# Optimization experiments

Hardware: AMD Instinct MI355X
Metric: run time of the kernel (lower is better)

The kernel has to match this reference:

```python
import jax, jax.numpy as jnp
import numpy as np

B, S, HID = 2, 2048, 2048
H = 16
Q_LORA = 1536
KV_LORA = 512
NOPE = 128
ROPE = 64
VDIM = 128
EPS = 1e-6
THETA = 10000.0
SCALE = 1.0 / np.sqrt(NOPE + ROPE)


def rmsnorm(x, w):
    var = jnp.mean(jnp.square(x), axis=-1, keepdims=True)
    return x * jax.lax.rsqrt(var + EPS) * w


def rotate_half(x):
    x1, x2 = jnp.split(x, 2, axis=-1)
    return jnp.concatenate([-x2, x1], axis=-1)


def setup_inputs() -> dict:
    key = jax.random.key(0)
    ks = jax.random.split(key, 10)
    w = 0.02
    hidden_states = jax.random.normal(ks[0], (B, S, HID), jnp.float32)
    # causal additive mask (bsz, 1, q_len, kv_len)
    causal = jnp.tril(jnp.ones((S, S), jnp.bool_))
    attention_mask = jnp.where(causal, 0.0, jnp.finfo(jnp.float32).min)[None, None].repeat(B, 0)
    position_ids = jnp.broadcast_to(jnp.arange(S, dtype=jnp.int64), (B, S))
    return {
        'hidden_states': hidden_states,
        'attention_mask': attention_mask,
        'q_a_w': jax.random.normal(ks[1], (Q_LORA, HID), jnp.float32) * w,
        'q_a_ln_w': jnp.ones((Q_LORA,), jnp.float32),
        'q_b_rope_w': jax.random.normal(ks[2], (H * ROPE, Q_LORA), jnp.float32) * w,
        'qk_nope_w': jax.random.normal(ks[3], (H * KV_LORA, Q_LORA), jnp.float32) * w,
        'kv_a_w': jax.random.normal(ks[4], (KV_LORA + ROPE, HID), jnp.float32) * w,
        'kv_a_ln_w': jnp.ones((KV_LORA,), jnp.float32),
        'v_b_w': jax.random.normal(ks[5], (H * VDIM, KV_LORA), jnp.float32) * w,
        'o_w': jax.random.normal(ks[6], (HID, H * VDIM), jnp.float32) * w,
        'position_ids': position_ids,
    }


def reference(hidden_states, attention_mask, q_a_w, q_a_ln_w, q_b_rope_w, qk_nope_w,
              kv_a_w, kv_a_ln_w, v_b_w, o_w, position_ids):
    b, s, _ = hidden_states.shape
    # low-rank Q path
    q_a = rmsnorm(hidden_states @ q_a_w.T, q_a_ln_w)                 # (b,s,Q_LORA)
    q_rope = (q_a @ q_b_rope_w.T).reshape(b, s, H, ROPE).transpose(0, 2, 1, 3)  # (b,h,s,rd)
    # compressed KV + shared rope key
    ckv_full = hidden_states @ kv_a_w.T                              # (b,s,KV_LORA+ROPE)
    ckv = rmsnorm(ckv_full[..., :KV_LORA], kv_a_ln_w)                # (b,s,KV_LORA)
    k_rope = ckv_full[..., KV_LORA:]                                 # (b,s,rd)
    # rotary embedding
    inv_freq = 1.0 / (THETA ** (jnp.arange(0, ROPE, 2, dtype=jnp.float32) / ROPE))
    t = jnp.arange(s, dtype=jnp.float32)
    freqs = jnp.outer(t, inv_freq)                                   # (s, rd/2)
    emb = jnp.concatenate([freqs, freqs], axis=-1)                   # (s, rd)
    cos = jnp.cos(emb)[position_ids][:, None]                        # (b,1,s,rd)
    sin = jnp.sin(emb)[position_ids][:, None]
    q_rope = q_rope * cos + rotate_half(q_rope) * sin                # (b,h,s,rd)
    k_rope = k_rope[:, None] * cos + rotate_half(k_rope[:, None]) * sin  # (b,1,s,rd)
    # absorbed nope score: q_a -> (b,h,s,KV_LORA) then vs compressed kv
    nope_q = (q_a @ qk_nope_w.T).reshape(b, s, H, KV_LORA).transpose(0, 2, 1, 3)
    nope_score = jnp.einsum('bhqc,bkc->bhqk', nope_q, ckv)
    rope_score = jnp.einsum('bhqr,bkr->bhqk', q_rope, k_rope[:, 0])
    attn = (nope_score + rope_score) * SCALE + attention_mask
    attn = jax.nn.softmax(attn.astype(jnp.float32), axis=-1).astype(hidden_states.dtype)
    # AV in compressed space, then absorbed v projection
    ctx = jnp.einsum('bhqk,bkc->bhqc', attn, ckv)                    # (b,h,q,KV_LORA)
    v_w = v_b_w.reshape(H, VDIM, KV_LORA)
    out = jnp.einsum('bhqc,hvc->bhqv', ctx, v_w)                     # (b,h,q,VDIM)
    out = out.transpose(0, 2, 1, 3).reshape(b, s, H * VDIM)
    return out @ o_w.T
```

## Files before the change

kernel.cpp:

```cpp
#include <hip/hip_runtime.h>
#include <hip/hip_bf16.h>

typedef __bf16 bf16;
typedef __bf16 bf16x8 __attribute__((ext_vector_type(8)));
typedef float f32x4 __attribute__((ext_vector_type(4)));
typedef float f32x16 __attribute__((ext_vector_type(16)));

#define AS3(p) ((__attribute__((address_space(3))) void*)(p))
#define AS1(p) ((const __attribute__((address_space(1))) void*)(p))
#define GLDS16(g,l) __builtin_amdgcn_global_load_lds(AS1(g), AS3(l), 16, 0, 0)
#define MFMA_BF16(a,b,c) __builtin_amdgcn_mfma_f32_16x16x32_bf16((a),(b),(c),0,0,0)
#define MFMA32(a,b,c) __builtin_amdgcn_mfma_f32_32x32x16_bf16((a),(b),(c),0,0,0)
#define SCHED_FENCE() do { __builtin_amdgcn_sched_barrier(0); asm volatile("" ::: "memory"); } while (0)

constexpr int S_ = 2048;
constexpr int H_ = 16;
constexpr int KVL_ = 512;
constexpr int ROPE_ = 64;
constexpr int VD_ = 128;
constexpr int DQK_ = 576;
constexpr int QKV_N = 2176;
constexpr float SCALE_ = 0.07216878364870323f;

__device__ __forceinline__ bf16 to_bf16(float f) {
    unsigned u = __builtin_bit_cast(unsigned, f);
    unsigned r = u + 0x7FFFu + ((u >> 16) & 1u);
    unsigned short h = (unsigned short)(r >> 16);
    return __builtin_bit_cast(bf16, h);
}

__device__ __forceinline__ unsigned short bf16bits(float f) {
    unsigned u = __builtin_bit_cast(unsigned, f);
    unsigned r = u + 0x7FFFu + ((u >> 16) & 1u);
    return (unsigned short)(r >> 16);
}

__device__ __forceinline__ unsigned cvt_pk_bf16(float lo, float hi) {
    unsigned r;
    asm("v_cvt_pk_bf16_f32 %0, %1, %2" : "=v"(r) : "v"(lo), "v"(hi));
    return r;
}

__global__ void cast_all_kernel(const float* __restrict__ s0, const float* __restrict__ s1,
                                const float* __restrict__ s2, const float* __restrict__ s3,
                                const float* __restrict__ s4, const float* __restrict__ s5,
                                const float* __restrict__ s6,
                                bf16* __restrict__ d0, bf16* __restrict__ d1, bf16* __restrict__ d2,
                                bf16* __restrict__ d3, bf16* __restrict__ d4, bf16* __restrict__ d5,
                                bf16* __restrict__ d6) {
    constexpr long ns[7]  = {8388608L, 3145728L, 1179648L, 1572864L, 12582912L, 1048576L, 4194304L};
    constexpr long pds[7] = {8388608L, 3145728L, 1310720L, 1572864L, 12582912L, 1048576L, 4194304L};
    const int seg = blockIdx.y;
    const float* in = (seg == 0) ? s0 : (seg == 1) ? s1 : (seg == 2) ? s2 : (seg == 3) ? s3
                    : (seg == 4) ? s4 : (seg == 5) ? s5 : s6;
    bf16* out = (seg == 0) ? d0 : (seg == 1) ? d1 : (seg == 2) ? d2 : (seg == 3) ? d3
              : (seg == 4) ? d4 : (seg == 5) ? d5 : d6;
    const long n = ns[seg], pad = pds[seg];
    long i = ((long)blockIdx.x * 256 + threadIdx.x) * 4;
    const long stride = (long)gridDim.x * 256 * 4;
    for (; i < pad; i += stride) {
        if (i < n) {
            float4 v = *(const float4*)(in + i);
            out[i + 0] = to_bf16(v.x); out[i + 1] = to_bf16(v.y);
            out[i + 2] = to_bf16(v.z); out[i + 3] = to_bf16(v.w);
        } else {
            out[i + 0] = to_bf16(0.f); out[i + 1] = to_bf16(0.f);
            out[i + 2] = to_bf16(0.f); out[i + 3] = to_bf16(0.f);
        }
    }
}

__global__ void rope_table_kernel(float* __restrict__ cosT, float* __restrict__ sinT) {
    int idx = blockIdx.x * 256 + threadIdx.x;
    if (idx >= S_ * 32) return;
    int s = idx >> 5, j = idx & 31;
    float invf = expf(-(float)(2 * j) * (1.0f / 64.0f) * 9.210340371976184f);
    float a = (float)s * invf;
    cosT[idx] = cosf(a);
    sinT[idx] = sinf(a);
}

__global__ void fused_post_kernel(const float* __restrict__ scr, const float* __restrict__ qw,
                                  const float* __restrict__ kw, const float* __restrict__ cosT,
                                  const float* __restrict__ sinT, bf16* __restrict__ qab,
                                  bf16* __restrict__ ckvb, bf16* __restrict__ krb) {
    const int row = blockIdx.x;
    const int tid = threadIdx.x;
    const float* x = scr + (long)row * QKV_N;
    float ssq = 0.f, ssk = 0.f;
    for (int i = tid; i < 1536; i += 256) { float v = x[i]; ssq += v * v; }
    for (int i = tid; i < 512; i += 256) { float v = x[1536 + i]; ssk += v * v; }
#pragma unroll
    for (int d = 1; d < 64; d <<= 1) { ssq += __shfl_xor(ssq, d); ssk += __shfl_xor(ssk, d); }
    __shared__ float rq[4], rk[4];
    if ((tid & 63) == 0) { rq[tid >> 6] = ssq; rk[tid >> 6] = ssk; }
    __syncthreads();
    float rsq = rsqrtf((rq[0] + rq[1] + rq[2] + rq[3]) / 1536.f + 1e-6f);
    float rsk = rsqrtf((rk[0] + rk[1] + rk[2] + rk[3]) / 512.f + 1e-6f);
    for (int i = tid; i < 1536; i += 256)
        qab[(long)row * 1536 + i] = to_bf16(x[i] * rsq * qw[i]);
    for (int i = tid; i < 512; i += 256)
        ckvb[(long)row * 512 + i] = to_bf16(x[1536 + i] * rsk * kw[i]);
    if (tid < 64) {
        int s = row & (S_ - 1);
        const float* kr = x + 2048;
        float other = (tid < 32) ? -kr[tid + 32] : kr[tid - 32];
        float c = cosT[s * 32 + (tid & 31)], sn = sinT[s * 32 + (tid & 31)];
        krb[(long)row * 64 + tid] = to_bf16(kr[tid] * c + other * sn);
    }
}

template <int MODE>
__global__ __launch_bounds__(256, 2)
void gemm_bt_kernel(const bf16* __restrict__ A, const bf16* __restrict__ Bm,
                    void* __restrict__ Cout, int M, int N, int K,
                    const float* __restrict__ cosT = nullptr,
                    const float* __restrict__ sinT = nullptr) {
    constexpr int BK = 32;
    __shared__ bf16 As[3][128 * BK];
    __shared__ bf16 Bs[3][128 * BK];
    const int tid = threadIdx.x;
    const int w = tid >> 6;
    const int lane = tid & 63;
    const int nwg = gridDim.x * gridDim.y;
    const int lin = blockIdx.y * gridDim.x + blockIdx.x;
    const int swz = (lin & 7) * (nwg >> 3) + (lin >> 3);
    const long m0 = (long)(swz % gridDim.x) * 128;
    const long n0 = (long)(swz / gridDim.x) * 128;
    const int wm = (w >> 1) * 64, wn = (w & 1) * 64;
    const int lr = lane & 15;
    const int lk = (lane >> 4) * 8;

    const int c0 = w * 2, c1 = w * 2 + 1;
    const int srow0 = c0 * 16 + (lane >> 2);
    const int srow1 = c1 * 16 + (lane >> 2);
    const int skc = (lane & 3) * 8;
    const bf16* ga0 = A + (m0 + srow0) * (long)K + skc;
    const bf16* ga1 = A + (m0 + srow1) * (long)K + skc;
    const bf16* gb0 = Bm + (n0 + srow0) * (long)K + skc;
    const bf16* gb1 = Bm + (n0 + srow1) * (long)K + skc;

#define GSTAGE(p) do { \
    GLDS16(ga0, &As[p][c0 * 512]); \
    GLDS16(gb0, &Bs[p][c0 * 512]); \
    GLDS16(ga1, &As[p][c1 * 512]); \
    GLDS16(gb1, &Bs[p][c1 * 512]); \
    ga0 += BK; ga1 += BK; gb0 += BK; gb1 += BK; \
} while (0)

    f32x4 acc[4][4] = {};
    const int nT = K / BK;

    GSTAGE(0);
    if (nT > 1) {
        GSTAGE(1);
        asm volatile("s_waitcnt vmcnt(4)" ::: "memory");
    } else {
        asm volatile("s_waitcnt vmcnt(0)" ::: "memory");
    }
    SCHED_FENCE();
    __builtin_amdgcn_s_barrier();
    SCHED_FENCE();

    for (int t = 0; t < nT; ++t) {
        const int p = t % 3;
        if (t + 2 < nT) GSTAGE((t + 2) % 3);
        bf16x8 av[4], bv[4];
#pragma unroll
        for (int i = 0; i < 4; i++) av[i] = *(const bf16x8*)&As[p][(wm + i * 16 + lr) * BK + lk];
#pragma unroll
        for (int j = 0; j < 4; j++) bv[j] = *(const bf16x8*)&Bs[p][(wn + j * 16 + lr) * BK + lk];
#pragma unroll
        for (int i = 0; i < 4; i++)
#pragma unroll
            for (int j = 0; j < 4; j++)
                acc[i][j] = MFMA_BF16(av[i], bv[j], acc[i][j]);
        if (t + 1 < nT) {
            SCHED_FENCE();
            if (t + 2 < nT) asm volatile("s_waitcnt vmcnt(4)" ::: "memory");
            else            asm volatile("s_waitcnt vmcnt(0)" ::: "memory");
            SCHED_FENCE();
            __builtin_amdgcn_s_barrier();
            SCHED_FENCE();
        }
    }
#undef GSTAGE

    const int r4 = (lane >> 4) * 4;
    if (MODE == 3) {
#pragma unroll
        for (int i = 0; i < 4; i++)
#pragma unroll
            for (int r = 0; r < 4; r++) {
                long gm = m0 + wm + i * 16 + r4 + r;
                int s = (int)(gm & (S_ - 1));
#pragma unroll
                for (int j = 0; j < 2; j++) {
                    float c = cosT[s * 32 + j * 16 + lr];
                    float sn = sinT[s * 32 + j * 16 + lr];
                    float lo = acc[i][j][r], hiv = acc[i][j + 2][r];
                    long gn = n0 + wn + j * 16 + lr;
                    ((bf16*)Cout)[gm * 1024 + gn] = to_bf16((lo * c - hiv * sn) * SCALE_);
                    ((bf16*)Cout)[gm * 1024 + gn + 32] = to_bf16((hiv * c + lo * sn) * SCALE_);
                }
            }
        return;
    }
#pragma unroll
    for (int i = 0; i < 4; i++)
#pragma unroll
        for (int j = 0; j < 4; j++) {
            long gmb = m0 + wm + i * 16 + r4;
            long gn = n0 + wn + j * 16 + lr;
            if (MODE == 2) {
                long idx = (gmb >> 11) * (2048L * 2048) + gn * 2048 + (gmb & 2047);
                ushort4 u;
                u.x = bf16bits(acc[i][j][0]);
                u.y = bf16bits(acc[i][j][1]);
                u.z = bf16bits(acc[i][j][2]);
                u.w = bf16bits(acc[i][j][3]);
                *(ushort4*)((bf16*)Cout + idx) = u;
            } else {
#pragma unroll
                for (int r = 0; r < 4; r++) {
                    long gm = gmb + r;
                    float v = acc[i][j][r];
                    if (MODE == 0) {
                        if (gn < N) ((float*)Cout)[gm * N + gn] = v;
                    } else {
                        if (gn < N) ((bf16*)Cout)[gm * N + gn] = to_bf16(v * SCALE_);
                    }
                }
            }
        }
}

__global__ __launch_bounds__(256, 2)
void flash_kernel(const bf16* __restrict__ nopeq, const bf16* __restrict__ ropeq,
                  const bf16* __restrict__ ckv, const bf16* __restrict__ krope,
                  const bf16* __restrict__ vt, bf16* __restrict__ outa) {
    __shared__ bf16 Ks2[32 * 512];
    __shared__ bf16 Krs[32 * 64];
    __shared__ char VtsB[10240];
    __shared__ char PldsB[4][32 * 80];
    const int tid = threadIdx.x;
    const int w = tid >> 6, lane = tid & 63;
    const int l31 = lane & 31;
    const int hi = lane >> 5;
    const int kel = hi * 8;
    const int klo = hi * 16;
    const int h = blockIdx.y, b = blockIdx.z;
    const int xq = (b == 0) ? (int)blockIdx.x : (15 - (int)blockIdx.x);
    const int q0 = xq * 128;
    const long bS = (long)b * S_;
    const int qg = q0 + (l31 << 2) + w;
    const int kvoff = hi * 4;

    bf16x8 qf[36];
    {
        const bf16* np = nopeq + (bS + qg) * (long)(H_ * KVL_) + h * KVL_;
        const bf16* rp = ropeq + (bS + qg) * (long)(H_ * ROPE_) + h * ROPE_;
#pragma unroll
        for (int t = 0; t < 32; ++t) qf[t] = *(const bf16x8*)(np + t * 16 + kel);
#pragma unroll
        for (int t = 0; t < 4; ++t) qf[32 + t] = *(const bf16x8*)(rp + t * 16 + kel);
    }

    unsigned soff[12];
#pragma unroll
    for (int k = 0; k < 8; ++k) {
        int c = w + 4 * k;
        soff[k] = (unsigned)((bS + c) * 1024 + ((lane * 16) ^ ((c & 7) << 4)));
    }
    {
        int rr = w * 8 + (lane >> 3);
        soff[8] = (unsigned)((bS + rr) * 128 + (((lane & 7) * 16) ^ ((rr & 7) << 4)));
    }
#pragma unroll
    for (int k = 9; k < 12; ++k) {
        int cc = (k == 11) ? (8 + w) : (w + 4 * (k - 9));
        int byt = cc * 1024 + lane * 16;
        int v = byt / 80, col = byt - v * 80;
        soff[k] = (col < 64) ? (unsigned)((((long)(b * H_ + h) * VD_ + v) * S_ + (col >> 1)) * 2) : 0u;
    }

    f32x16 accv[4] = {};
    float m_run = -3e38f, l_run = 0.f;
    const int nkv = q0 / 32 + 4;
    const int kswz = (l31 & 7) << 4;

    for (int it = 0; it < nkv; ++it) {
        const int kv0 = it * 32;
        __syncthreads();
#pragma unroll
        for (int k = 0; k < 8; ++k) {
            GLDS16((const char*)ckv + soff[k], (char*)Ks2 + (w + 4 * k) * 1024);
            soff[k] += 32768;
        }
        GLDS16((const char*)krope + soff[8], (char*)Krs + w * 1024);
        soff[8] += 4096;
        GLDS16((const char*)vt + soff[9], VtsB + w * 1024); soff[9] += 64;
        GLDS16((const char*)vt + soff[10], VtsB + (w + 4) * 1024); soff[10] += 64;
        if (w < 2) { GLDS16((const char*)vt + soff[11], VtsB + (8 + w) * 1024); soff[11] += 64; }
        __syncthreads();

        f32x16 sc = {};
        __builtin_amdgcn_s_setprio(1);
#pragma unroll
        for (int t = 0; t < 32; ++t) {
            bf16x8 kf = *(const bf16x8*)((const char*)Ks2 + l31 * 1024 + ((t * 32 + klo) ^ kswz));
            sc = MFMA32(kf, qf[t], sc);
        }
#pragma unroll
        for (int t = 0; t < 4; ++t) {
            bf16x8 kf = *(const bf16x8*)((const char*)Krs + l31 * 128 + ((t * 32 + klo) ^ kswz));
            sc = MFMA32(kf, qf[32 + t], sc);
        }
        __builtin_amdgcn_s_setprio(0);

        float s[16];
        if (kv0 + 31 > q0 + w) {
#pragma unroll
            for (int r = 0; r < 16; ++r) {
                int kvg = kv0 + kvoff + ((r & 3) + 8 * (r >> 2));
                s[r] = (kvg > qg) ? -3e38f : sc[r];
            }
        } else {
#pragma unroll
            for (int r = 0; r < 16; ++r) s[r] = sc[r];
        }

        float m8[8];
#pragma unroll
        for (int r = 0; r < 8; ++r) m8[r] = fmaxf(s[r], s[r + 8]);
        float m4a = fmaxf(m8[0], m8[1]), m4b = fmaxf(m8[2], m8[3]);
        float m4c = fmaxf(m8[4], m8[5]), m4d = fmaxf(m8[6], m8[7]);
        float mx = fmaxf(fmaxf(m4a, m4b), fmaxf(m4c, m4d));
        mx = fmaxf(mx, __shfl_xor(mx, 32));

        float mnew = fmaxf(m_run, mx);
        float corr = __expf(m_run - mnew);
#pragma unroll
        for (int r = 0; r < 16; ++r) s[r] = __expf(s[r] - mnew);
        float r8[8];
#pragma unroll
        for (int r = 0; r < 8; ++r) r8[r] = s[r] + s[r + 8];
        float r4a = r8[0] + r8[1], r4b = r8[2] + r8[3], r4c = r8[4] + r8[5], r4d = r8[6] + r8[7];
        float rs = (r4a + r4b) + (r4c + r4d);
        rs += __shfl_xor(rs, 32);

        if (__any(mnew > m_run)) {
#pragma unroll
            for (int vg = 0; vg < 4; ++vg)
#pragma unroll
                for (int r = 0; r < 16; ++r) accv[vg][r] *= corr;
        }
        l_run = l_run * corr + rs;
        m_run = mnew;

        {
            char* prow = PldsB[w] + l31 * 80;
#pragma unroll
            for (int g = 0; g < 4; ++g) {
                uint2 pk;
                pk.x = cvt_pk_bf16(s[4 * g + 0], s[4 * g + 1]);
                pk.y = cvt_pk_bf16(s[4 * g + 2], s[4 * g + 3]);
                *(uint2*)(prow + g * 16 + 8 * hi) = pk;
            }
        }
        bf16x8 pfrag[2];
#pragma unroll
        for (int c = 0; c < 2; ++c)
            pfrag[c] = *(const bf16x8*)(PldsB[w] + l31 * 80 + c * 32 + klo);

        __builtin_amdgcn_s_setprio(1);
#pragma unroll
        for (int c = 0; c < 2; ++c) {
#pragma unroll
            for (int vg = 0; vg < 4; ++vg) {
                bf16x8 vf = *(const bf16x8*)(VtsB + (vg * 32 + l31) * 80 + c * 32 + klo);
                accv[vg] = MFMA32(vf, pfrag[c], accv[vg]);
            }
        }
        __builtin_amdgcn_s_setprio(0);
    }

    float invl = 1.f / l_run;
    bf16* orow = outa + (bS + qg) * (long)(H_ * VD_) + h * VD_;
#pragma unroll
    for (int vg = 0; vg < 4; ++vg)
#pragma unroll
        for (int rq = 0; rq < 4; ++rq) {
            int vb = vg * 32 + rq * 8 + kvoff;
            ushort4 u;
            u.x = __builtin_bit_cast(unsigned short, to_bf16(accv[vg][rq * 4 + 0] * invl));
            u.y = __builtin_bit_cast(unsigned short, to_bf16(accv[vg][rq * 4 + 1] * invl));
            u.z = __builtin_bit_cast(unsigned short, to_bf16(accv[vg][rq * 4 + 2] * invl));
            u.w = __builtin_bit_cast(unsigned short, to_bf16(accv[vg][rq * 4 + 3] * invl));
            *(ushort4*)(orow + vb) = u;
        }
}

extern "C" void kernel_launch(void* const* d_in, const int* in_sizes, int n_in,
                              void* d_out, int out_size, void* d_ws, size_t ws_size,
                              hipStream_t stream) {
    const float* hidden     = (const float*)d_in[0];
    const float* q_a_w      = (const float*)d_in[2];
    const float* q_a_ln_w   = (const float*)d_in[3];
    const float* q_b_rope_w = (const float*)d_in[4];
    const float* qk_nope_w  = (const float*)d_in[5];
    const float* kv_a_w     = (const float*)d_in[6];
    const float* kv_a_ln_w  = (const float*)d_in[7];
    const float* v_b_w      = (const float*)d_in[8];
    const float* o_w        = (const float*)d_in[9];

    char* ws = (char*)d_ws;
    size_t off = 0;
    auto alloc = [&](size_t bytes) -> void* {
        void* p = ws + off;
        off += (bytes + 255) & ~(size_t)255;
        return p;
    };
    bf16* hb     = (bf16*)alloc(4096L * 2048 * 2);
    bf16* wqakv  = (bf16*)alloc((long)QKV_N * 2048 * 2);
    bf16* wqr    = (bf16*)alloc(1024L * 1536 * 2);
    bf16* wnp    = (bf16*)alloc(8192L * 1536 * 2);
    bf16* wvb    = (bf16*)alloc(2048L * 512 * 2);
    bf16* wo     = (bf16*)alloc(2048L * 2048 * 2);
    float* f32scr = (float*)alloc(4096L * QKV_N * 4);
    bf16* qab    = (bf16*)alloc(4096L * 1536 * 2);
    bf16* qrb    = (bf16*)alloc(4096L * 1024 * 2);
    bf16* npq    = (bf16*)alloc(4096L * 8192 * 2);
    bf16* ckvb   = (bf16*)alloc(4096L * 512 * 2);
    bf16* krb    = (bf16*)alloc(4096L * 64 * 2);
    bf16* vtb    = (bf16*)alloc(2L * 2048 * 2048 * 2);
    bf16* aout   = (bf16*)alloc(4096L * 2048 * 2);
    float* cosT  = (float*)alloc(2048L * 32 * 4);
    float* sinT  = (float*)alloc(2048L * 32 * 4);
    (void)ws_size; (void)in_sizes; (void)n_in; (void)out_size;

    cast_all_kernel<<<dim3(512, 7), 256, 0, stream>>>(
        hidden, q_a_w, kv_a_w, q_b_rope_w, qk_nope_w, v_b_w, o_w,
        hb, wqakv, wqakv + 1536L * 2048, wqr, wnp, wvb, wo);
    rope_table_kernel<<<256, 256, 0, stream>>>(cosT, sinT);

    gemm_bt_kernel<0><<<dim3(32, 17), 256, 0, stream>>>(hb, wqakv, f32scr, 4096, QKV_N, 2048);
    fused_post_kernel<<<4096, 256, 0, stream>>>(f32scr, q_a_ln_w, kv_a_ln_w, cosT, sinT, qab, ckvb, krb);
    gemm_bt_kernel<3><<<dim3(32, 8), 256, 0, stream>>>(qab, wqr, qrb, 4096, 1024, 1536, cosT, sinT);
    gemm_bt_kernel<1><<<dim3(32, 64), 256, 0, stream>>>(qab, wnp, npq, 4096, 8192, 1536);
    gemm_bt_kernel<2><<<dim3(32, 16), 256, 0, stream>>>(ckvb, wvb, vtb, 4096, 2048, 512);
    flash_kernel<<<dim3(16, 16, 2), 256, 0, stream>>>(npq, qrb, ckvb, krb, vtb, aout);
    gemm_bt_kernel<0><<<dim3(32, 16), 256, 0, stream>>>(aout, wo, (float*)d_out, 4096, 2048, 2048);
}
```

Measured before the change: 589.9 us.

## Add 256x256-tile triple-buffered GEMM for the absorbed nope-Q projection

Adds a new GEMM kernel with 256x256 output tiles, 512 threads, and a three-stage LDS pipeline fed by direct global-to-LDS loads with XOR swizzling and grid swizzling. It replaces the previous 128-tile GEMM for the largest projection (4096x8192x1536). The intent is to raise arithmetic intensity and data reuse per workgroup and to hide load latency. In exchange the kernel runs one block per CU, and its epilogue writes bf16 elements one at a time without vectorized stores.

After: 589.5 us. No clear change (-0.1%).

```diff
diff --git a/kernel.cpp b/kernel.cpp
--- a/kernel.cpp
+++ b/kernel.cpp
@@ -235,6 +235,100 @@
         }
 }
 
+template <int MODE>
+__global__ __launch_bounds__(512, 1)
+void gemm256_kernel(const bf16* __restrict__ A, const bf16* __restrict__ Bm,
+                    void* __restrict__ Cout, int M, int N, int K) {
+    constexpr int BK = 32;
+    __shared__ bf16 As[3][256 * BK];
+    __shared__ bf16 Bs[3][256 * BK];
+    const int tid = threadIdx.x;
+    const int w = tid >> 6, lane = tid & 63;
+    const int wr = w >> 2, wc = w & 3;
+    const int nwg = gridDim.x * gridDim.y;
+    const int lin = blockIdx.y * gridDim.x + blockIdx.x;
+    const int swz = (lin & 7) * (nwg >> 3) + (lin >> 3);
+    const long m0 = (long)(swz % gridDim.x) * 256;
+    const long n0 = (long)(swz / gridDim.x) * 256;
+    const int lr = lane & 15;
+    const int lg = lane >> 4;
+
+    const int srow = tid >> 2;
+    const int sce = ((tid & 3) * 8) ^ ((srow & 3) << 3);
+    const bf16* gA0 = A + (m0 + srow) * (long)K + sce;
+    const bf16* gA1 = A + (m0 + 128 + srow) * (long)K + sce;
+    const bf16* gB0 = Bm + (n0 + srow) * (long)K + sce;
+    const bf16* gB1 = Bm + (n0 + 128 + srow) * (long)K + sce;
+
+#define GSTAGE2(p) do { \
+    GLDS16(gA0, (char*)&As[p][0] + tid * 16); \
+    GLDS16(gA1, (char*)&As[p][0] + 8192 + tid * 16); \
+    GLDS16(gB0, (char*)&Bs[p][0] + tid * 16); \
+    GLDS16(gB1, (char*)&Bs[p][0] + 8192 + tid * 16); \
+    gA0 += BK; gA1 += BK; gB0 += BK; gB1 += BK; \
+} while (0)
+
+    f32x4 acc[8][4] = {};
+    const int nT = K / BK;
+
+    const int rcol = (lg * 16) ^ ((lr & 3) << 4);
+
+    GSTAGE2(0);
+    if (nT > 1) {
+        GSTAGE2(1);
+        asm volatile("s_waitcnt vmcnt(4)" ::: "memory");
+    } else {
+        asm volatile("s_waitcnt vmcnt(0)" ::: "memory");
+    }
+    SCHED_FENCE();
+    __builtin_amdgcn_s_barrier();
+    SCHED_FENCE();
+
+    for (int t = 0; t < nT; ++t) {
+        const int p = t % 3;
+        if (t + 2 < nT) GSTAGE2((t + 2) % 3);
+        bf16x8 av[8], bv[4];
+#pragma unroll
+        for (int i = 0; i < 8; i++)
+            av[i] = *(const bf16x8*)((const char*)&As[p][0] + (wr * 128 + i * 16 + lr) * 64 + rcol);
+#pragma unroll
+        for (int j = 0; j < 4; j++)
+            bv[j] = *(const bf16x8*)((const char*)&Bs[p][0] + (wc * 64 + j * 16 + lr) * 64 + rcol);
+        __builtin_amdgcn_s_setprio(1);
+#pragma unroll
+        for (int i = 0; i < 8; i++)
+#pragma unroll
+            for (int j = 0; j < 4; j++)
+                acc[i][j] = MFMA_BF16(av[i], bv[j], acc[i][j]);
+        __builtin_amdgcn_s_setprio(0);
+        if (t + 1 < nT) {
+            SCHED_FENCE();
+            if (t + 2 < nT) asm volatile("s_waitcnt vmcnt(4)" ::: "memory");
+            else            asm volatile("s_waitcnt vmcnt(0)" ::: "memory");
+            SCHED_FENCE();
+            __builtin_amdgcn_s_barrier();
+            SCHED_FENCE();
+        }
+    }
+#undef GSTAGE2
+
+    const int r4 = lg * 4;
+#pragma unroll
+    for (int i = 0; i < 8; i++)
+#pragma unroll
+        for (int j = 0; j < 4; j++) {
+            long gmb = m0 + wr * 128 + i * 16 + r4;
+            long gn = n0 + wc * 64 + j * 16 + lr;
+#pragma unroll
+            for (int r = 0; r < 4; r++) {
+                long gm = gmb + r;
+                float v = acc[i][j][r];
+                if (MODE == 0) ((float*)Cout)[gm * N + gn] = v;
+                else           ((bf16*)Cout)[gm * N + gn] = to_bf16(v * SCALE_);
+            }
+        }
+}
+
 __global__ __launch_bounds__(256, 2)
 void flash_kernel(const bf16* __restrict__ nopeq, const bf16* __restrict__ ropeq,
                   const bf16* __restrict__ ckv, const bf16* __restrict__ krope,
@@ -447,7 +541,7 @@
     gemm_bt_kernel<0><<<dim3(32, 17), 256, 0, stream>>>(hb, wqakv, f32scr, 4096, QKV_N, 2048);
     fused_post_kernel<<<4096, 256, 0, stream>>>(f32scr, q_a_ln_w, kv_a_ln_w, cosT, sinT, qab, ckvb, krb);
     gemm_bt_kernel<3><<<dim3(32, 8), 256, 0, stream>>>(qab, wqr, qrb, 4096, 1024, 1536, cosT, sinT);
-    gemm_bt_kernel<1><<<dim3(32, 64), 256, 0, stream>>>(qab, wnp, npq, 4096, 8192, 1536);
+    gemm256_kernel<1><<<dim3(16, 32), 512, 0, stream>>>(qab, wnp, npq, 4096, 8192, 1536);
     gemm_bt_kernel<2><<<dim3(32, 16), 256, 0, stream>>>(ckvb, wvb, vtb, 4096, 2048, 512);
     flash_kernel<<<dim3(16, 16, 2), 256, 0, stream>>>(npq, qrb, ckvb, krb, vtb, aout);
     gemm_bt_kernel<0><<<dim3(32, 16), 256, 0, stream>>>(aout, wo, (float*)d_out, 4096, 2048, 2048);
```

## Add 256x256 eight-wave pipelined GEMM for the nope-query projection

Applied to the files above, without the earlier changes.

Adds a new 512-thread GEMM kernel with 256x256 output tiles, double-buffered swizzled LDS staged through global_load_lds, and phase-interleaved loads with barriers and setprio around the MFMA blocks. It replaces the generic GEMM for the largest projection (4096x8192x1536). The aim is more data reuse per tile and better overlap of memory loads with MFMA work. In exchange it runs at one block per CU with heavy register use, and stores output element by element without vectorisation.

New measurement: 556.3 us. 1.06x faster.

```diff
diff --git a/kernel.cpp b/kernel.cpp
--- a/kernel.cpp
+++ b/kernel.cpp
@@ -235,6 +235,116 @@
         }
 }
 
+template <int MODE>
+__global__ __launch_bounds__(512, 1)
+void gemm8p_kernel(const bf16* __restrict__ A, const bf16* __restrict__ Bm,
+                   void* __restrict__ Cout, int M, int N, int K) {
+    __shared__ bf16 Abuf[2][256 * 64];
+    __shared__ bf16 Bbuf[2][256 * 64];
+    const int tid = threadIdx.x;
+    const int w = tid >> 6, lane = tid & 63;
+    const int wr = w >> 2, wc = w & 3;
+    const int lr = lane & 15, lg = lane >> 4;
+    const int nwg = gridDim.x * gridDim.y;
+    const int lin = blockIdx.y * gridDim.x + blockIdx.x;
+    const int swz = (lin & 7) * (nwg >> 3) + (lin >> 3);
+    const long m0 = (long)(swz % gridDim.x) * 256;
+    const long n0 = (long)(swz / gridDim.x) * 256;
+
+    const int rbase = tid >> 3;
+    const int clb = (tid & 7) * 16;
+    const int elem0 = (clb ^ ((rbase & 7) << 4)) >> 1;
+    const int dstoff = rbase * 128 + clb;
+    const bf16* pA = A + (m0 + rbase) * (long)K + elem0;
+    const bf16* pB = Bm + (n0 + rbase) * (long)K + elem0;
+    const int nK = K / 64;
+
+#define STG8(isB, buf, kt, h) do { \
+    const bf16* _s = ((isB) ? pB : pA) + (long)((h) * 128) * K + (kt) * 64; \
+    char* _d = (char*)((isB) ? &Bbuf[buf][0] : &Abuf[buf][0]) + (h) * 16384 + dstoff; \
+    GLDS16(_s, _d); \
+    GLDS16(_s + 64L * K, _d + 8192); \
+} while (0)
+
+    const int rsw = (lr & 7) << 4;
+#define ARD8(buf, i, kk) (*(const bf16x8*)((const char*)&Abuf[buf][0] + (wr * 128 + (i) * 16 + lr) * 128 + ((((kk) * 64) + lg * 16) ^ rsw)))
+#define BRD8(buf, j, kk) (*(const bf16x8*)((const char*)&Bbuf[buf][0] + (wc * 64 + (j) * 16 + lr) * 128 + ((((kk) * 64) + lg * 16) ^ rsw)))
+
+    f32x4 acc[8][4] = {};
+    bf16x8 bv0[4], bv1[4];
+
+    STG8(0, 0, 0, 0); STG8(0, 0, 0, 1);
+    STG8(1, 0, 0, 0); STG8(1, 0, 0, 1);
+    STG8(1, 1, 1, 0); STG8(1, 1, 1, 1);
+    SCHED_FENCE();
+    asm volatile("s_waitcnt vmcnt(4)" ::: "memory");
+    SCHED_FENCE();
+    __builtin_amdgcn_s_barrier();
+    SCHED_FENCE();
+
+#define PHASE8(BUF, Q, STAGE_STMT, ENDWAIT_STMT) do { \
+    bf16x8 a00 = ARD8(BUF, 2 * (Q), 0), a01 = ARD8(BUF, 2 * (Q), 1); \
+    bf16x8 a10 = ARD8(BUF, 2 * (Q) + 1, 0), a11 = ARD8(BUF, 2 * (Q) + 1, 1); \
+    if ((Q) == 0) { \
+        _Pragma("unroll") \
+        for (int j = 0; j < 4; ++j) { bv0[j] = BRD8(BUF, j, 0); bv1[j] = BRD8(BUF, j, 1); } \
+    } \
+    STAGE_STMT; \
+    SCHED_FENCE(); \
+    __builtin_amdgcn_s_barrier(); \
+    SCHED_FENCE(); \
+    __builtin_amdgcn_s_setprio(1); \
+    _Pragma("unroll") \
+    for (int j = 0; j < 4; ++j) { \
+        acc[2 * (Q)][j]     = MFMA_BF16(a00, bv0[j], acc[2 * (Q)][j]); \
+        acc[2 * (Q)][j]     = MFMA_BF16(a01, bv1[j], acc[2 * (Q)][j]); \
+        acc[2 * (Q) + 1][j] = MFMA_BF16(a10, bv0[j], acc[2 * (Q) + 1][j]); \
+        acc[2 * (Q) + 1][j] = MFMA_BF16(a11, bv1[j], acc[2 * (Q) + 1][j]); \
+    } \
+    __builtin_amdgcn_s_setprio(0); \
+    SCHED_FENCE(); \
+    ENDWAIT_STMT; \
+    SCHED_FENCE(); \
+    __builtin_amdgcn_s_barrier(); \
+    SCHED_FENCE(); \
+} while (0)
+
+    const int nIter = nK / 2;
+    for (int it = 0; it < nIter; ++it) {
+        const int kt0 = 2 * it, kt1 = kt0 + 1;
+        PHASE8(0, 0, STG8(0, 1, kt1, 0), (void)0);
+        PHASE8(0, 1, STG8(0, 1, kt1, 1), (void)0);
+        PHASE8(0, 2, if (kt0 + 2 < nK) STG8(1, 0, kt0 + 2, 0), (void)0);
+        PHASE8(0, 3, if (kt0 + 2 < nK) STG8(1, 0, kt0 + 2, 1),
+               asm volatile("s_waitcnt vmcnt(4)" ::: "memory"));
+        PHASE8(1, 0, if (kt0 + 2 < nK) STG8(0, 0, kt0 + 2, 0), (void)0);
+        PHASE8(1, 1, if (kt0 + 2 < nK) STG8(0, 0, kt0 + 2, 1), (void)0);
+        PHASE8(1, 2, if (kt1 + 2 < nK) STG8(1, 1, kt1 + 2, 0), (void)0);
+        PHASE8(1, 3, if (kt1 + 2 < nK) STG8(1, 1, kt1 + 2, 1),
+               asm volatile("s_waitcnt vmcnt(4)" ::: "memory"));
+    }
+#undef PHASE8
+#undef STG8
+#undef ARD8
+#undef BRD8
+
+    const int r4 = lg * 4;
+#pragma unroll
+    for (int i = 0; i < 8; i++)
+#pragma unroll
+        for (int j = 0; j < 4; j++) {
+            long gmb = m0 + wr * 128 + i * 16 + r4;
+            long gn = n0 + wc * 64 + j * 16 + lr;
+#pragma unroll
+            for (int r = 0; r < 4; r++) {
+                long gm = gmb + r;
+                float v = acc[i][j][r];
+                if (MODE == 0) ((float*)Cout)[gm * N + gn] = v;
+                else           ((bf16*)Cout)[gm * N + gn] = to_bf16(v * SCALE_);
+            }
+        }
+}
+
 __global__ __launch_bounds__(256, 2)
 void flash_kernel(const bf16* __restrict__ nopeq, const bf16* __restrict__ ropeq,
                   const bf16* __restrict__ ckv, const bf16* __restrict__ krope,
@@ -447,7 +557,7 @@
     gemm_bt_kernel<0><<<dim3(32, 17), 256, 0, stream>>>(hb, wqakv, f32scr, 4096, QKV_N, 2048);
     fused_post_kernel<<<4096, 256, 0, stream>>>(f32scr, q_a_ln_w, kv_a_ln_w, cosT, sinT, qab, ckvb, krb);
     gemm_bt_kernel<3><<<dim3(32, 8), 256, 0, stream>>>(qab, wqr, qrb, 4096, 1024, 1536, cosT, sinT);
-    gemm_bt_kernel<1><<<dim3(32, 64), 256, 0, stream>>>(qab, wnp, npq, 4096, 8192, 1536);
+    gemm8p_kernel<1><<<dim3(16, 32), 512, 0, stream>>>(qab, wnp, npq, 4096, 8192, 1536);
     gemm_bt_kernel<2><<<dim3(32, 16), 256, 0, stream>>>(ckvb, wvb, vtb, 4096, 2048, 512);
     flash_kernel<<<dim3(16, 16, 2), 256, 0, stream>>>(npq, qrb, ckvb, krb, vtb, aout);
     gemm_bt_kernel<0><<<dim3(32, 16), 256, 0, stream>>>(aout, wo, (float*)d_out, 4096, 2048, 2048);
```
